# Kernel optimization log

Hardware: AMD Instinct MI355X
Metric: run time of the kernel (lower is better)

Reference implementation:

```python
import jax, jax.numpy as jnp
import numpy as np

T, B, I, H = 2048, 4096, 3, 5  # seq_len, batch, input_size, hidden_size (from module)


def setup_inputs() -> dict:
    key = jax.random.key(0)
    ks = jax.random.split(key, 10)
    k = 1.0 / np.sqrt(H)  # torch nn.RNN default init bound
    u = lambda kk, shape: jax.random.uniform(kk, shape, jnp.float32, -k, k)
    return {
        "x": jax.random.normal(ks[0], (T, B, I), jnp.float32),
        "hx": jax.random.normal(ks[1], (2, B, H), jnp.float32),
        "w_ih0": u(ks[2], (H, I)),
        "w_hh0": u(ks[3], (H, H)),
        "b_ih0": u(ks[4], (H,)),
        "b_hh0": u(ks[5], (H,)),
        "w_ih1": u(ks[6], (H, H)),
        "w_hh1": u(ks[7], (H, H)),
        "b_ih1": u(ks[8], (H,)),
        "b_hh1": u(ks[9], (H,)),
    }


def reference(x, hx, w_ih0, w_hh0, b_ih0, b_hh0, w_ih1, w_hh1, b_ih1, b_hh1):
    # Precompute layer-0 input projections for all timesteps in one big GEMM.
    pre0 = jnp.einsum("tbi,hi->tbh", x, w_ih0) + b_ih0  # [T, B, H]

    def step(carry, p0_t):
        h0, h1 = carry
        h0 = jnp.tanh(p0_t + h0 @ w_hh0.T + b_hh0)
        h1 = jnp.tanh(h0 @ w_ih1.T + b_ih1 + h1 @ w_hh1.T + b_hh1)
        return (h0, h1), h1

    (h0_f, h1_f), out = jax.lax.scan(step, (hx[0], hx[1]), pre0)
    h_n = jnp.stack([h0_f, h1_f])  # [2, B, H]
    return out, h_n
```

## Files before the change

kernel.cpp:

```cpp
#include <hip/hip_runtime.h>


typedef float v2f  __attribute__((ext_vector_type(2)));
typedef float v2fu __attribute__((ext_vector_type(2), aligned(4)));
typedef float v3fu __attribute__((ext_vector_type(3), aligned(4)));

#define SEQ_T 2048
#define BATCH 4096
#define ISZ 3
#define HSZ 5
#define XSTRIDE (BATCH * ISZ)
#define OSTRIDE (BATCH * HSZ)

template<int K>
__device__ __forceinline__ float qbcast(float v) {
    return __int_as_float(__builtin_amdgcn_mov_dpp(
        __float_as_int(v), K * 0x55, 0xF, 0xF, false));
}
__device__ __forceinline__ v2f vsplat(float s) { return (v2f){s, s}; }
__device__ __forceinline__ v2f vfma(float s, v2f w, v2f a) {
    return __builtin_elementwise_fma(vsplat(s), w, a);
}

__global__ __launch_bounds__(64, 1)
void rnn2_diet(const float* __restrict__ x, const float* __restrict__ hx,
               const float* __restrict__ w_ih0, const float* __restrict__ w_hh0,
               const float* __restrict__ b_ih0, const float* __restrict__ b_hh0,
               const float* __restrict__ w_ih1, const float* __restrict__ w_hh1,
               const float* __restrict__ b_ih1, const float* __restrict__ b_hh1,
               float* __restrict__ out)
{
    const int tid = threadIdx.x;
    const int c   = (blockIdx.x * 64 + tid) >> 2;
    const int ja  = tid & 3;
    const int jb  = ja + 1;
    const float S = 2.8853900817779268f;

    const v2f bias0p = (v2f){ S * (b_ih0[ja] + b_hh0[ja]), S * (b_ih0[jb] + b_hh0[jb]) };
    const v2f bias1p = (v2f){ S * (b_ih1[ja] + b_hh1[ja]), S * (b_ih1[jb] + b_hh1[jb]) };
#define LW(W, k, n)  (v2f){ S * W[ja * (n) + (k)], S * W[jb * (n) + (k)] }
    const v2f wi0p0 = LW(w_ih0, 0, ISZ), wi0p1 = LW(w_ih0, 1, ISZ), wi0p2 = LW(w_ih0, 2, ISZ);
    const v2f wh0p0 = LW(w_hh0, 0, HSZ), wh0p1 = LW(w_hh0, 1, HSZ), wh0p2 = LW(w_hh0, 2, HSZ),
              wh0p3 = LW(w_hh0, 3, HSZ), wh0p4 = LW(w_hh0, 4, HSZ);
    const v2f wi1p0 = LW(w_ih1, 0, HSZ), wi1p1 = LW(w_ih1, 1, HSZ), wi1p2 = LW(w_ih1, 2, HSZ),
              wi1p3 = LW(w_ih1, 3, HSZ), wi1p4 = LW(w_ih1, 4, HSZ);
    const v2f wh1p0 = LW(w_hh1, 0, HSZ), wh1p1 = LW(w_hh1, 1, HSZ), wh1p2 = LW(w_hh1, 2, HSZ),
              wh1p3 = LW(w_hh1, 3, HSZ), wh1p4 = LW(w_hh1, 4, HSZ);
#undef LW

    float h0b0 = hx[(size_t)c * HSZ + 0], h0b1 = hx[(size_t)c * HSZ + 1],
          h0b2 = hx[(size_t)c * HSZ + 2], h0b3 = hx[(size_t)c * HSZ + 3],
          h0b4 = hx[(size_t)c * HSZ + 4];
    const size_t hb1 = (size_t)BATCH * HSZ + (size_t)c * HSZ;
    float h1b0 = hx[hb1 + 0], h1b1 = hx[hb1 + 1], h1b2 = hx[hb1 + 2],
          h1b3 = hx[hb1 + 3], h1b4 = hx[hb1 + 4];

    unsigned xoff = (unsigned)c * ISZ;
    v3fu x0 = *(const v3fu*)(x + xoff + 0*XSTRIDE);
    v3fu x1 = *(const v3fu*)(x + xoff + 1*XSTRIDE);
    v3fu x2 = *(const v3fu*)(x + xoff + 2*XSTRIDE);
    v3fu x3 = *(const v3fu*)(x + xoff + 3*XSTRIDE);
    v3fu x4 = *(const v3fu*)(x + xoff + 4*XSTRIDE);
    v3fu x5 = *(const v3fu*)(x + xoff + 5*XSTRIDE);
    v3fu x6 = *(const v3fu*)(x + xoff + 6*XSTRIDE);
    v3fu x7 = *(const v3fu*)(x + xoff + 7*XSTRIDE);
    xoff += 8 * XSTRIDE;

    unsigned ooff = (unsigned)c * HSZ + (unsigned)ja;

#define PAIR(XV, DOLOAD)                                                   \
    {                                                                      \
        const float xv0 = XV.x, xv1 = XV.y, xv2 = XV.z;                    \
        if (DOLOAD) {                                                      \
            XV = *(const v3fu*)(x + xoff);                                 \
            xoff += XSTRIDE;                                               \
        }                                                                  \
        v2f a = bias0p, cc = (v2f){0.0f, 0.0f};                            \
        v2f d = bias1p, ee = (v2f){0.0f, 0.0f};                            \
        a  = vfma(xv0,  wi0p0, a);                                         \
        d  = vfma(h0b0, wi1p0, d);                                         \
        cc = vfma(xv1,  wi0p1, cc);                                        \
        ee = vfma(h0b1, wi1p1, ee);                                        \
        a  = vfma(xv2,  wi0p2, a);                                         \
        d  = vfma(h0b2, wi1p2, d);                                         \
        cc = vfma(h0b0, wh0p0, cc);                                        \
        ee = vfma(h0b3, wi1p3, ee);                                        \
        a  = vfma(h0b1, wh0p1, a);                                         \
        d  = vfma(h0b4, wi1p4, d);                                         \
        cc = vfma(h0b2, wh0p2, cc);                                        \
        ee = vfma(h1b0, wh1p0, ee);                                        \
        a  = vfma(h0b3, wh0p3, a);                                         \
        d  = vfma(h1b1, wh1p1, d);                                         \
        cc = vfma(h0b4, wh0p4, cc);                                        \
        ee = vfma(h1b2, wh1p2, ee);                                        \
        a = a + cc;                                                        \
        d  = vfma(h1b3, wh1p3, d);                                         \
        ee = vfma(h1b4, wh1p4, ee);                                        \
        v2f e0;                                                            \
        e0.x = __builtin_amdgcn_exp2f(a.x);                                \
        e0.y = __builtin_amdgcn_exp2f(a.y);                                \
        d = d + ee;                                                        \
        v2f e1;                                                            \
        e1.x = __builtin_amdgcn_exp2f(d.x);                                \
        e1.y = __builtin_amdgcn_exp2f(d.y);                                \
        const v2f p0 = e0 + vsplat(1.0f);                                  \
        const v2f p1 = e1 + vsplat(1.0f);                                  \
        v2f r0;                                                            \
        r0.x = __builtin_amdgcn_rcpf(p0.x);                                \
        r0.y = __builtin_amdgcn_rcpf(p0.y);                                \
        v2f r1;                                                            \
        r1.x = __builtin_amdgcn_rcpf(p1.x);                                \
        r1.y = __builtin_amdgcn_rcpf(p1.y);                                \
        const v2f n0 = __builtin_elementwise_fma(vsplat(-2.0f), r0, vsplat(1.0f)); \
        const v2f n1 = __builtin_elementwise_fma(vsplat(-2.0f), r1, vsplat(1.0f)); \
        h0b0 = qbcast<0>(n0.x);                                            \
        h0b1 = qbcast<1>(n0.x);                                            \
        h0b2 = qbcast<2>(n0.x);                                            \
        h0b3 = qbcast<3>(n0.x);                                            \
        h0b4 = qbcast<3>(n0.y);                                            \
        *(v2fu*)(out + ooff) = n1;                                         \
        ooff += OSTRIDE;                                                   \
        h1b0 = qbcast<0>(n1.x);                                            \
        h1b1 = qbcast<1>(n1.x);                                            \
        h1b2 = qbcast<2>(n1.x);                                            \
        h1b3 = qbcast<3>(n1.x);                                            \
        h1b4 = qbcast<3>(n1.y);                                            \
    }

#define P0ONLY(XV)                                                         \
    {                                                                      \
        const float xv0 = XV.x, xv1 = XV.y, xv2 = XV.z;                    \
        XV = *(const v3fu*)(x + xoff);                                     \
        xoff += XSTRIDE;                                                   \
        v2f a = bias0p, cc = (v2f){0.0f, 0.0f};                            \
        a  = vfma(xv0,  wi0p0, a);                                         \
        cc = vfma(xv1,  wi0p1, cc);                                        \
        a  = vfma(xv2,  wi0p2, a);                                         \
        cc = vfma(h0b0, wh0p0, cc);                                        \
        a  = vfma(h0b1, wh0p1, a);                                         \
        cc = vfma(h0b2, wh0p2, cc);                                        \
        a  = vfma(h0b3, wh0p3, a);                                         \
        cc = vfma(h0b4, wh0p4, cc);                                        \
        a = a + cc;                                                        \
        v2f e0;                                                            \
        e0.x = __builtin_amdgcn_exp2f(a.x);                                \
        e0.y = __builtin_amdgcn_exp2f(a.y);                                \
        const v2f p0 = e0 + vsplat(1.0f);                                  \
        v2f r0;                                                            \
        r0.x = __builtin_amdgcn_rcpf(p0.x);                                \
        r0.y = __builtin_amdgcn_rcpf(p0.y);                                \
        const v2f n0 = __builtin_elementwise_fma(vsplat(-2.0f), r0, vsplat(1.0f)); \
        h0b0 = qbcast<0>(n0.x);                                            \
        h0b1 = qbcast<1>(n0.x);                                            \
        h0b2 = qbcast<2>(n0.x);                                            \
        h0b3 = qbcast<3>(n0.x);                                            \
        h0b4 = qbcast<3>(n0.y);                                            \
    }

    P0ONLY(x0)
    PAIR(x1, 1)
    PAIR(x2, 1)
    PAIR(x3, 1)
    PAIR(x4, 1)
    PAIR(x5, 1)
    PAIR(x6, 1)
    PAIR(x7, 1)

    for (int blk = 1; blk < SEQ_T / 8 - 1; ++blk) {
        PAIR(x0, 1)
        PAIR(x1, 1)
        PAIR(x2, 1)
        PAIR(x3, 1)
        PAIR(x4, 1)
        PAIR(x5, 1)
        PAIR(x6, 1)
        PAIR(x7, 1)
    }

    PAIR(x0, 0)
    PAIR(x1, 0)
    PAIR(x2, 0)
    PAIR(x3, 0)
    PAIR(x4, 0)
    PAIR(x5, 0)
    PAIR(x6, 0)
    PAIR(x7, 0)

    {
        v2f d = bias1p, ee = (v2f){0.0f, 0.0f};
        d  = vfma(h0b0, wi1p0, d);
        ee = vfma(h0b1, wi1p1, ee);
        d  = vfma(h0b2, wi1p2, d);
        ee = vfma(h0b3, wi1p3, ee);
        d  = vfma(h0b4, wi1p4, d);
        ee = vfma(h1b0, wh1p0, ee);
        d  = vfma(h1b1, wh1p1, d);
        ee = vfma(h1b2, wh1p2, ee);
        d  = vfma(h1b3, wh1p3, d);
        ee = vfma(h1b4, wh1p4, ee);
        d = d + ee;
        v2f e1;
        e1.x = __builtin_amdgcn_exp2f(d.x);
        e1.y = __builtin_amdgcn_exp2f(d.y);
        const v2f p1 = e1 + vsplat(1.0f);
        v2f r1;
        r1.x = __builtin_amdgcn_rcpf(p1.x);
        r1.y = __builtin_amdgcn_rcpf(p1.y);
        const v2f n1 = __builtin_elementwise_fma(vsplat(-2.0f), r1, vsplat(1.0f));
        *(v2fu*)(out + ooff) = n1;
        h1b0 = qbcast<0>(n1.x);
        h1b1 = qbcast<1>(n1.x);
        h1b2 = qbcast<2>(n1.x);
        h1b3 = qbcast<3>(n1.x);
        h1b4 = qbcast<3>(n1.y);
    }
#undef PAIR
#undef P0ONLY

    float* hn = out + (size_t)SEQ_T * BATCH * HSZ;
    hn[(size_t)c * HSZ + 0] = h0b0;
    hn[(size_t)c * HSZ + 1] = h0b1;
    hn[(size_t)c * HSZ + 2] = h0b2;
    hn[(size_t)c * HSZ + 3] = h0b3;
    hn[(size_t)c * HSZ + 4] = h0b4;
    hn[hb1 + 0] = h1b0;
    hn[hb1 + 1] = h1b1;
    hn[hb1 + 2] = h1b2;
    hn[hb1 + 3] = h1b3;
    hn[hb1 + 4] = h1b4;
}

extern "C" void kernel_launch(void* const* d_in, const int* in_sizes, int n_in,
                              void* d_out, int out_size, void* d_ws, size_t ws_size,
                              hipStream_t stream) {
    rnn2_diet<<<(BATCH * 4) / 64, 64, 0, stream>>>(
        (const float*)d_in[0], (const float*)d_in[1],
        (const float*)d_in[2], (const float*)d_in[3],
        (const float*)d_in[4], (const float*)d_in[5],
        (const float*)d_in[6], (const float*)d_in[7],
        (const float*)d_in[8], (const float*)d_in[9],
        (float*)d_out);
}
```

Baseline: 424.5 us.

## Map each batch row to 8 lanes with scalar math and ds_swizzle broadcast

Each batch element now uses 8 lanes, one hidden unit per lane, with lanes 5-7 clamped to unit 4 and doing redundant work. The old layout used 4 lanes with two packed units each. The per-lane recurrence becomes scalar FMAs instead of packed v2f ops. The hidden-state broadcast switches from quad DPP moves to ds_swizzle within groups of 8. The intent is to shorten the per-step serial dependency chain by halving the work per lane, at the cost of twice as many waves, wasted lanes, and ds_swizzle latency, which is higher than DPP.

```diff
diff --git a/kernel.cpp b/kernel.cpp
--- a/kernel.cpp
+++ b/kernel.cpp
@@ -1,8 +1,6 @@
 #include <hip/hip_runtime.h>
 
 
-typedef float v2f  __attribute__((ext_vector_type(2)));
-typedef float v2fu __attribute__((ext_vector_type(2), aligned(4)));
 typedef float v3fu __attribute__((ext_vector_type(3), aligned(4)));
 
 #define SEQ_T 2048
@@ -13,40 +11,34 @@
 #define OSTRIDE (BATCH * HSZ)
 
 template<int K>
-__device__ __forceinline__ float qbcast(float v) {
-    return __int_as_float(__builtin_amdgcn_mov_dpp(
-        __float_as_int(v), K * 0x55, 0xF, 0xF, false));
+__device__ __forceinline__ float sw8(float v) {
+    return __int_as_float(__builtin_amdgcn_ds_swizzle(
+        __float_as_int(v), (K << 5) | 0x18));
 }
-__device__ __forceinline__ v2f vsplat(float s) { return (v2f){s, s}; }
-__device__ __forceinline__ v2f vfma(float s, v2f w, v2f a) {
-    return __builtin_elementwise_fma(vsplat(s), w, a);
-}
 
 __global__ __launch_bounds__(64, 1)
-void rnn2_diet(const float* __restrict__ x, const float* __restrict__ hx,
-               const float* __restrict__ w_ih0, const float* __restrict__ w_hh0,
-               const float* __restrict__ b_ih0, const float* __restrict__ b_hh0,
-               const float* __restrict__ w_ih1, const float* __restrict__ w_hh1,
-               const float* __restrict__ b_ih1, const float* __restrict__ b_hh1,
-               float* __restrict__ out)
+void rnn2_sc8(const float* __restrict__ x, const float* __restrict__ hx,
+              const float* __restrict__ w_ih0, const float* __restrict__ w_hh0,
+              const float* __restrict__ b_ih0, const float* __restrict__ b_hh0,
+              const float* __restrict__ w_ih1, const float* __restrict__ w_hh1,
+              const float* __restrict__ b_ih1, const float* __restrict__ b_hh1,
+              float* __restrict__ out)
 {
     const int tid = threadIdx.x;
-    const int c   = (blockIdx.x * 64 + tid) >> 2;
-    const int ja  = tid & 3;
-    const int jb  = ja + 1;
+    const int c   = (blockIdx.x * 64 + tid) >> 3;
+    const int l   = tid & 7;
+    const int j   = (l < HSZ) ? l : (HSZ - 1);
     const float S = 2.8853900817779268f;
 
-    const v2f bias0p = (v2f){ S * (b_ih0[ja] + b_hh0[ja]), S * (b_ih0[jb] + b_hh0[jb]) };
-    const v2f bias1p = (v2f){ S * (b_ih1[ja] + b_hh1[ja]), S * (b_ih1[jb] + b_hh1[jb]) };
-#define LW(W, k, n)  (v2f){ S * W[ja * (n) + (k)], S * W[jb * (n) + (k)] }
-    const v2f wi0p0 = LW(w_ih0, 0, ISZ), wi0p1 = LW(w_ih0, 1, ISZ), wi0p2 = LW(w_ih0, 2, ISZ);
-    const v2f wh0p0 = LW(w_hh0, 0, HSZ), wh0p1 = LW(w_hh0, 1, HSZ), wh0p2 = LW(w_hh0, 2, HSZ),
-              wh0p3 = LW(w_hh0, 3, HSZ), wh0p4 = LW(w_hh0, 4, HSZ);
-    const v2f wi1p0 = LW(w_ih1, 0, HSZ), wi1p1 = LW(w_ih1, 1, HSZ), wi1p2 = LW(w_ih1, 2, HSZ),
-              wi1p3 = LW(w_ih1, 3, HSZ), wi1p4 = LW(w_ih1, 4, HSZ);
-    const v2f wh1p0 = LW(w_hh1, 0, HSZ), wh1p1 = LW(w_hh1, 1, HSZ), wh1p2 = LW(w_hh1, 2, HSZ),
-              wh1p3 = LW(w_hh1, 3, HSZ), wh1p4 = LW(w_hh1, 4, HSZ);
-#undef LW
+    const float bias0 = S * (b_ih0[j] + b_hh0[j]);
+    const float bias1 = S * (b_ih1[j] + b_hh1[j]);
+    const float wi00 = S * w_ih0[j*ISZ+0], wi01 = S * w_ih0[j*ISZ+1], wi02 = S * w_ih0[j*ISZ+2];
+    const float wh00 = S * w_hh0[j*HSZ+0], wh01 = S * w_hh0[j*HSZ+1], wh02 = S * w_hh0[j*HSZ+2],
+                wh03 = S * w_hh0[j*HSZ+3], wh04 = S * w_hh0[j*HSZ+4];
+    const float wi10 = S * w_ih1[j*HSZ+0], wi11 = S * w_ih1[j*HSZ+1], wi12 = S * w_ih1[j*HSZ+2],
+                wi13 = S * w_ih1[j*HSZ+3], wi14 = S * w_ih1[j*HSZ+4];
+    const float wh10 = S * w_hh1[j*HSZ+0], wh11 = S * w_hh1[j*HSZ+1], wh12 = S * w_hh1[j*HSZ+2],
+                wh13 = S * w_hh1[j*HSZ+3], wh14 = S * w_hh1[j*HSZ+4];
 
     float h0b0 = hx[(size_t)c * HSZ + 0], h0b1 = hx[(size_t)c * HSZ + 1],
           h0b2 = hx[(size_t)c * HSZ + 2], h0b3 = hx[(size_t)c * HSZ + 3],
@@ -66,7 +58,7 @@
     v3fu x7 = *(const v3fu*)(x + xoff + 7*XSTRIDE);
     xoff += 8 * XSTRIDE;
 
-    unsigned ooff = (unsigned)c * HSZ + (unsigned)ja;
+    unsigned ooff = (unsigned)c * HSZ + (unsigned)j;
 
 #define PAIR(XV, DOLOAD)                                                   \
     {                                                                      \
@@ -75,56 +67,46 @@
             XV = *(const v3fu*)(x + xoff);                                 \
             xoff += XSTRIDE;                                               \
         }                                                                  \
-        v2f a = bias0p, cc = (v2f){0.0f, 0.0f};                            \
-        v2f d = bias1p, ee = (v2f){0.0f, 0.0f};                            \
-        a  = vfma(xv0,  wi0p0, a);                                         \
-        d  = vfma(h0b0, wi1p0, d);                                         \
-        cc = vfma(xv1,  wi0p1, cc);                                        \
-        ee = vfma(h0b1, wi1p1, ee);                                        \
-        a  = vfma(xv2,  wi0p2, a);                                         \
-        d  = vfma(h0b2, wi1p2, d);                                         \
-        cc = vfma(h0b0, wh0p0, cc);                                        \
-        ee = vfma(h0b3, wi1p3, ee);                                        \
-        a  = vfma(h0b1, wh0p1, a);                                         \
-        d  = vfma(h0b4, wi1p4, d);                                         \
-        cc = vfma(h0b2, wh0p2, cc);                                        \
-        ee = vfma(h1b0, wh1p0, ee);                                        \
-        a  = vfma(h0b3, wh0p3, a);                                         \
-        d  = vfma(h1b1, wh1p1, d);                                         \
-        cc = vfma(h0b4, wh0p4, cc);                                        \
-        ee = vfma(h1b2, wh1p2, ee);                                        \
+        float a = bias0, cc = 0.0f;                                        \
+        float d = bias1, ee = 0.0f;                                        \
+        a  = fmaf(xv0,  wi00, a);                                          \
+        d  = fmaf(h0b0, wi10, d);                                          \
+        cc = fmaf(xv1,  wi01, cc);                                         \
+        ee = fmaf(h0b1, wi11, ee);                                         \
+        a  = fmaf(xv2,  wi02, a);                                          \
+        d  = fmaf(h0b2, wi12, d);                                          \
+        cc = fmaf(h0b0, wh00, cc);                                         \
+        ee = fmaf(h0b3, wi13, ee);                                         \
+        a  = fmaf(h0b1, wh01, a);                                          \
+        d  = fmaf(h0b4, wi14, d);                                          \
+        cc = fmaf(h0b2, wh02, cc);                                         \
+        ee = fmaf(h1b0, wh10, ee);                                         \
+        a  = fmaf(h0b3, wh03, a);                                          \
+        d  = fmaf(h1b1, wh11, d);                                          \
+        cc = fmaf(h0b4, wh04, cc);                                         \
+        ee = fmaf(h1b2, wh12, ee);                                         \
         a = a + cc;                                                        \
-        d  = vfma(h1b3, wh1p3, d);                                         \
-        ee = vfma(h1b4, wh1p4, ee);                                        \
-        v2f e0;                                                            \
-        e0.x = __builtin_amdgcn_exp2f(a.x);                                \
-        e0.y = __builtin_amdgcn_exp2f(a.y);                                \
+        d  = fmaf(h1b3, wh13, d);                                          \
+        ee = fmaf(h1b4, wh14, ee);                                         \
+        const float e0 = __builtin_amdgcn_exp2f(a);                        \
         d = d + ee;                                                        \
-        v2f e1;                                                            \
-        e1.x = __builtin_amdgcn_exp2f(d.x);                                \
-        e1.y = __builtin_amdgcn_exp2f(d.y);                                \
-        const v2f p0 = e0 + vsplat(1.0f);                                  \
-        const v2f p1 = e1 + vsplat(1.0f);                                  \
-        v2f r0;                                                            \
-        r0.x = __builtin_amdgcn_rcpf(p0.x);                                \
-        r0.y = __builtin_amdgcn_rcpf(p0.y);                                \
-        v2f r1;                                                            \
-        r1.x = __builtin_amdgcn_rcpf(p1.x);                                \
-        r1.y = __builtin_amdgcn_rcpf(p1.y);                                \
-        const v2f n0 = __builtin_elementwise_fma(vsplat(-2.0f), r0, vsplat(1.0f)); \
-        const v2f n1 = __builtin_elementwise_fma(vsplat(-2.0f), r1, vsplat(1.0f)); \
-        h0b0 = qbcast<0>(n0.x);                                            \
-        h0b1 = qbcast<1>(n0.x);                                            \
-        h0b2 = qbcast<2>(n0.x);                                            \
-        h0b3 = qbcast<3>(n0.x);                                            \
-        h0b4 = qbcast<3>(n0.y);                                            \
-        *(v2fu*)(out + ooff) = n1;                                         \
+        const float e1 = __builtin_amdgcn_exp2f(d);                        \
+        const float r0 = __builtin_amdgcn_rcpf(1.0f + e0);                 \
+        const float r1 = __builtin_amdgcn_rcpf(1.0f + e1);                 \
+        const float n0 = fmaf(-2.0f, r0, 1.0f);                           \
+        const float n1 = fmaf(-2.0f, r1, 1.0f);                           \
+        h0b0 = sw8<0>(n0);                                                 \
+        h0b1 = sw8<1>(n0);                                                 \
+        h0b2 = sw8<2>(n0);                                                 \
+        h0b3 = sw8<3>(n0);                                                 \
+        h0b4 = sw8<4>(n0);                                                 \
+        out[ooff] = n1;                                                    \
         ooff += OSTRIDE;                                                   \
-        h1b0 = qbcast<0>(n1.x);                                            \
-        h1b1 = qbcast<1>(n1.x);                                            \
-        h1b2 = qbcast<2>(n1.x);                                            \
-        h1b3 = qbcast<3>(n1.x);                                            \
-        h1b4 = qbcast<3>(n1.y);                                            \
+        h1b0 = sw8<0>(n1);                                                 \
+        h1b1 = sw8<1>(n1);                                                 \
+        h1b2 = sw8<2>(n1);                                                 \
+        h1b3 = sw8<3>(n1);                                                 \
+        h1b4 = sw8<4>(n1);                                                 \
     }
 
 #define P0ONLY(XV)                                                         \
@@ -132,29 +114,24 @@
         const float xv0 = XV.x, xv1 = XV.y, xv2 = XV.z;                    \
         XV = *(const v3fu*)(x + xoff);                                     \
         xoff += XSTRIDE;                                                   \
-        v2f a = bias0p, cc = (v2f){0.0f, 0.0f};                            \
-        a  = vfma(xv0,  wi0p0, a);                                         \
-        cc = vfma(xv1,  wi0p1, cc);                                        \
-        a  = vfma(xv2,  wi0p2, a);                                         \
-        cc = vfma(h0b0, wh0p0, cc);                                        \
-        a  = vfma(h0b1, wh0p1, a);                                         \
-        cc = vfma(h0b2, wh0p2, cc);                                        \
-        a  = vfma(h0b3, wh0p3, a);                                         \
-        cc = vfma(h0b4, wh0p4, cc);                                        \
+        float a = bias0, cc = 0.0f;                                        \
+        a  = fmaf(xv0,  wi00, a);                                          \
+        cc = fmaf(xv1,  wi01, cc);                                         \
+        a  = fmaf(xv2,  wi02, a);                                          \
+        cc = fmaf(h0b0, wh00, cc);                                         \
+        a  = fmaf(h0b1, wh01, a);                                          \
+        cc = fmaf(h0b2, wh02, cc);                                         \
+        a  = fmaf(h0b3, wh03, a);                                          \
+        cc = fmaf(h0b4, wh04, cc);                                         \
         a = a + cc;                                                        \
-        v2f e0;                                                            \
-        e0.x = __builtin_amdgcn_exp2f(a.x);                                \
-        e0.y = __builtin_amdgcn_exp2f(a.y);                                \
-        const v2f p0 = e0 + vsplat(1.0f);                                  \
-        v2f r0;                                                            \
-        r0.x = __builtin_amdgcn_rcpf(p0.x);                                \
-        r0.y = __builtin_amdgcn_rcpf(p0.y);                                \
-        const v2f n0 = __builtin_elementwise_fma(vsplat(-2.0f), r0, vsplat(1.0f)); \
-        h0b0 = qbcast<0>(n0.x);                                            \
-        h0b1 = qbcast<1>(n0.x);                                            \
-        h0b2 = qbcast<2>(n0.x);                                            \
-        h0b3 = qbcast<3>(n0.x);                                            \
-        h0b4 = qbcast<3>(n0.y);                                            \
+        const float e0 = __builtin_amdgcn_exp2f(a);                        \
+        const float r0 = __builtin_amdgcn_rcpf(1.0f + e0);                 \
+        const float n0 = fmaf(-2.0f, r0, 1.0f);                           \
+        h0b0 = sw8<0>(n0);                                                 \
+        h0b1 = sw8<1>(n0);                                                 \
+        h0b2 = sw8<2>(n0);                                                 \
+        h0b3 = sw8<3>(n0);                                                 \
+        h0b4 = sw8<4>(n0);                                                 \
     }
 
     P0ONLY(x0)
@@ -187,32 +164,27 @@
     PAIR(x7, 0)
 
     {
-        v2f d = bias1p, ee = (v2f){0.0f, 0.0f};
-        d  = vfma(h0b0, wi1p0, d);
-        ee = vfma(h0b1, wi1p1, ee);
-        d  = vfma(h0b2, wi1p2, d);
-        ee = vfma(h0b3, wi1p3, ee);
-        d  = vfma(h0b4, wi1p4, d);
-        ee = vfma(h1b0, wh1p0, ee);
-        d  = vfma(h1b1, wh1p1, d);
-        ee = vfma(h1b2, wh1p2, ee);
-        d  = vfma(h1b3, wh1p3, d);
-        ee = vfma(h1b4, wh1p4, ee);
+        float d = bias1, ee = 0.0f;
+        d  = fmaf(h0b0, wi10, d);
+        ee = fmaf(h0b1, wi11, ee);
+        d  = fmaf(h0b2, wi12, d);
+        ee = fmaf(h0b3, wi13, ee);
+        d  = fmaf(h0b4, wi14, d);
+        ee = fmaf(h1b0, wh10, ee);
+        d  = fmaf(h1b1, wh11, d);
+        ee = fmaf(h1b2, wh12, ee);
+        d  = fmaf(h1b3, wh13, d);
+        ee = fmaf(h1b4, wh14, ee);
         d = d + ee;
-        v2f e1;
-        e1.x = __builtin_amdgcn_exp2f(d.x);
-        e1.y = __builtin_amdgcn_exp2f(d.y);
-        const v2f p1 = e1 + vsplat(1.0f);
-        v2f r1;
-        r1.x = __builtin_amdgcn_rcpf(p1.x);
-        r1.y = __builtin_amdgcn_rcpf(p1.y);
-        const v2f n1 = __builtin_elementwise_fma(vsplat(-2.0f), r1, vsplat(1.0f));
-        *(v2fu*)(out + ooff) = n1;
-        h1b0 = qbcast<0>(n1.x);
-        h1b1 = qbcast<1>(n1.x);
-        h1b2 = qbcast<2>(n1.x);
-        h1b3 = qbcast<3>(n1.x);
-        h1b4 = qbcast<3>(n1.y);
+        const float e1 = __builtin_amdgcn_exp2f(d);
+        const float r1 = __builtin_amdgcn_rcpf(1.0f + e1);
+        const float n1 = fmaf(-2.0f, r1, 1.0f);
+        out[ooff] = n1;
+        h1b0 = sw8<0>(n1);
+        h1b1 = sw8<1>(n1);
+        h1b2 = sw8<2>(n1);
+        h1b3 = sw8<3>(n1);
+        h1b4 = sw8<4>(n1);
     }
 #undef PAIR
 #undef P0ONLY
@@ -233,7 +205,7 @@
 extern "C" void kernel_launch(void* const* d_in, const int* in_sizes, int n_in,
                               void* d_out, int out_size, void* d_ws, size_t ws_size,
                               hipStream_t stream) {
-    rnn2_diet<<<(BATCH * 4) / 64, 64, 0, stream>>>(
+    rnn2_sc8<<<(BATCH * 8) / 64, 64, 0, stream>>>(
         (const float*)d_in[0], (const float*)d_in[1],
         (const float*)d_in[2], (const float*)d_in[3],
         (const float*)d_in[4], (const float*)d_in[5],
```

After: 532.2 us. +25.4%, slower.
